# Performance work log

Hardware: AMD Instinct MI355X
Metric: run time of the kernel (lower is better)

## Reference

```python
import jax, jax.numpy as jnp
import numpy as np

N = 20000      # nodes
E = 320000     # edges (before self loops)
HID = 128      # args.hidden
HEADS = 8
C1 = HID // 2  # 64, gat1 out per head -> 512 concat
C2 = HID // 4  # 32, gat2 out per head -> 256 concat
D1 = HEADS * C1  # 512
D2 = HEADS * C2  # 256
JKD = HID + D1 + D2  # 896


def _glorot(key, shape):
    fan_in, fan_out = shape[0], shape[-1]
    s = jnp.sqrt(6.0 / (fan_in + fan_out))
    return jax.random.uniform(key, shape, jnp.float32, -s, s)


def setup_inputs() -> dict:
    key = jax.random.key(0)
    ks = jax.random.split(key, 18)
    x = jax.random.normal(ks[0], (N, HID), jnp.float32)
    edge_index = jax.random.randint(ks[1], (2, E), 0, N, dtype=jnp.int32)
    return {
        "x": x,
        "edge_index": edge_index,
        # GATv2 layer 1
        "Wl1": _glorot(ks[2], (HID, D1)), "bl1": jnp.zeros((D1,), jnp.float32),
        "Wr1": _glorot(ks[3], (HID, D1)), "br1": jnp.zeros((D1,), jnp.float32),
        "att1": _glorot(ks[4], (HEADS, C1)),
        "bias1": jnp.zeros((D1,), jnp.float32),
        # GATv2 layer 2
        "Wl2": _glorot(ks[5], (D1, D2)), "bl2": jnp.zeros((D2,), jnp.float32),
        "Wr2": _glorot(ks[6], (D1, D2)), "br2": jnp.zeros((D2,), jnp.float32),
        "att2": _glorot(ks[7], (HEADS, C2)),
        "bias2": jnp.zeros((D2,), jnp.float32),
        # JK linear
        "Wjk": _glorot(ks[8], (JKD, HID)), "bjk": jnp.zeros((HID,), jnp.float32),
    }


def gatv2_layer(x, src, dst, Wl, bl, Wr, br, att, bias, n):
    """PyG GATv2Conv (concat=True, eval mode: no dropout), neg_slope=0.2."""
    H, C = att.shape
    xl = (x @ Wl + bl).reshape(n, H, C)  # source transform (messages)
    xr = (x @ Wr + br).reshape(n, H, C)  # target transform
    e = jax.nn.leaky_relu(xl[src] + xr[dst], 0.2)        # [E,H,C]
    logits = jnp.einsum('ehc,hc->eh', e, att)            # [E,H]
    # numerically stable segment softmax over incoming edges per dst node
    m = jax.ops.segment_max(logits, dst, num_segments=n) # [N,H]
    a = jnp.exp(logits - m[dst])
    denom = jax.ops.segment_sum(a, dst, num_segments=n)
    alpha = a / denom[dst]                               # [E,H]
    out = jax.ops.segment_sum(alpha[:, :, None] * xl[src], dst, num_segments=n)
    return out.reshape(n, H * C) + bias


def reference(x, edge_index, Wl1, bl1, Wr1, br1, att1, bias1,
              Wl2, bl2, Wr2, br2, att2, bias2, Wjk, bjk):
    n = x.shape[0]
    loop = jnp.arange(n, dtype=edge_index.dtype)
    src = jnp.concatenate([edge_index[0], loop])  # add self loops (PyG default)
    dst = jnp.concatenate([edge_index[1], loop])

    jk0 = x
    h1 = jax.nn.elu(gatv2_layer(x, src, dst, Wl1, bl1, Wr1, br1, att1, bias1, n))
    h2 = jax.nn.elu(gatv2_layer(h1, src, dst, Wl2, bl2, Wr2, br2, att2, bias2, n))
    jk = jnp.concatenate([jk0, h1, h2], axis=-1)  # JumpingKnowledge('cat')
    return jk @ Wjk + bjk
```

## Files before the change

kernel.cpp:

```cpp
#include <hip/hip_runtime.h>

typedef unsigned short u16;
typedef __attribute__((ext_vector_type(8))) short bf16x8;
typedef __attribute__((ext_vector_type(4))) float f32x4;

__device__ __forceinline__ float bf2f(u16 u) { return __uint_as_float(((unsigned)u) << 16); }
__device__ __forceinline__ u16 f2bf(float f) {
  unsigned u = __float_as_uint(f);
  u += 0x7fffu + ((u >> 16) & 1u);
  return (u16)(u >> 16);
}
__device__ __forceinline__ void bf2x2(unsigned w, float& lo, float& hi) {
  lo = __uint_as_float(w << 16);
  hi = __uint_as_float(w & 0xffff0000u);
}

__device__ __forceinline__ float red8(float p) {
  p += __int_as_float(__builtin_amdgcn_ds_swizzle(__float_as_int(p), 0x041F));
  p += __int_as_float(__builtin_amdgcn_ds_swizzle(__float_as_int(p), 0x081F));
  p += __int_as_float(__builtin_amdgcn_ds_swizzle(__float_as_int(p), 0x101F));
  return p;
}

__global__ __launch_bounds__(256) void prep_kernel(
    const float* __restrict__ x,
    const float* __restrict__ bl1, const float* __restrict__ br1,
    const float* __restrict__ bl2, const float* __restrict__ br2,
    u16* __restrict__ XH, float* __restrict__ BC1, float* __restrict__ BC2,
    int* __restrict__ cur,
    int nx, int total)
{
  int i = blockIdx.x * 256 + threadIdx.x;
  if (i >= total) return;
  if (i < nx) { XH[i] = f2bf(x[i]); return; }
  int j = i - nx;
  if (j < 1024) { BC1[j] = (j < 512) ? bl1[j] : br1[j - 512]; return; }
  if (j < 1536) { int t = j - 1024; BC2[t] = (t < 256) ? bl2[t] : br2[t - 256]; return; }
  cur[j - 1536] = 0;
}

__global__ __launch_bounds__(256) void wtrans_kernel(
    const float* __restrict__ Wl1, const float* __restrict__ Wr1,
    const float* __restrict__ Wl2, const float* __restrict__ Wr2,
    const float* __restrict__ Wjk,
    u16* __restrict__ Wp)
{
  __shared__ float T[64][65];
  int t = blockIdx.x;
  const float *Wa, *Wb; int Nhalf, lds, k0, n0, KsT, SUBS; size_t obase; bool split;
  if (t < 32) {
    int kt = t & 1, nt = t >> 1;
    k0 = kt * 64; n0 = nt * 64; obase = 0; KsT = 4; SUBS = 8; split = true;
    Wa = Wl1; Wb = Wr1; Nhalf = 512; lds = 512;
  } else if (t < 96) {
    int tt = t - 32; int kt = tt & 7, nt = tt >> 3;
    k0 = kt * 64; n0 = nt * 64; obase = 262144; KsT = 16; SUBS = 8; split = true;
    Wa = Wl2; Wb = Wr2; Nhalf = 256; lds = 256;
  } else {
    int tt = t - 96; int kt = tt % 14, nt = tt / 14;
    k0 = kt * 64; n0 = nt * 64; obase = 786432; KsT = 28; SUBS = 4; split = false;
    Wa = Wjk; Wb = nullptr; Nhalf = 128; lds = 128;
  }
  const int tid = threadIdx.x;
  const int lane = tid & 63, unit = tid >> 6;
  {
    int n = n0 + lane;
    const float* S = (n < Nhalf) ? Wa : Wb;
    int nn = (n < Nhalf) ? n : n - Nhalf;
#pragma unroll
    for (int r = 0; r < 16; ++r) {
      int kl = unit + 4 * r;
      T[kl][lane] = S[(size_t)(k0 + kl) * lds + nn];
    }
  }
  __syncthreads();
  const int tn = n0 >> 6;
#pragma unroll
  for (int u = 0; u < 2; ++u) {
    int c = unit * 2 + u;
    int ks_l = c >> 2, nc = c & 3;
    int ksg = (k0 >> 5) + ks_l;
    size_t ob = obase + ((size_t)(tn * KsT + ksg) * SUBS + nc) * 512 + lane * 8;
#pragma unroll
    for (int j = 0; j < 8; ++j) {
      float v = T[ks_l * 32 + (lane >> 4) * 8 + j][nc * 16 + (lane & 15)];
      u16 h = f2bf(v);
      Wp[ob + j] = h;
      if (split) Wp[ob + 2048 + j] = f2bf(v - bf2f(h));
    }
  }
}

__global__ __launch_bounds__(256) void hist_kernel(
    const int* __restrict__ ei, int E, int ET, int* __restrict__ cnt)
{
  int e = blockIdx.x * 256 + threadIdx.x;
  if (e >= ET) return;
  int d = (e < E) ? ei[E + e] : (e - E);
  atomicAdd(&cnt[d], 1);
}

__global__ __launch_bounds__(1024) void scan_kernel(
    int* __restrict__ cnt, int* __restrict__ rowptr, int n)
{
  __shared__ int wsum[16];
  __shared__ int carry;
  const int tid = threadIdx.x, lane = tid & 63, wv = tid >> 6;
  if (tid == 0) carry = 0;
  __syncthreads();
  for (int base = 0; base < n; base += 1024) {
    int i = base + tid;
    int v = (i < n) ? cnt[i] : 0;
    if (i < n) cnt[i] = 0;
    int s = v;
#pragma unroll
    for (int ofs = 1; ofs < 64; ofs <<= 1) {
      int t = __shfl_up(s, ofs);
      if (lane >= ofs) s += t;
    }
    if (lane == 63) wsum[wv] = s;
    __syncthreads();
    if (wv == 0 && lane < 16) {
      int t = wsum[lane];
#pragma unroll
      for (int ofs = 1; ofs < 16; ofs <<= 1) {
        int u = __shfl_up(t, ofs);
        if (lane >= ofs) t += u;
      }
      wsum[lane] = t;
    }
    __syncthreads();
    int waveoff = (wv == 0) ? 0 : wsum[wv - 1];
    if (i < n) rowptr[i] = carry + waveoff + s - v;
    int tot = wsum[15];
    __syncthreads();
    if (tid == 0) carry += tot;
    __syncthreads();
  }
  if (threadIdx.x == 0) rowptr[n] = carry;
}

__global__ __launch_bounds__(256) void scatter_kernel(
    const int* __restrict__ ei, int E, int ET,
    const int* __restrict__ rowptr, int* __restrict__ cur, int* __restrict__ srcs)
{
  int e = blockIdx.x * 256 + threadIdx.x;
  if (e >= ET) return;
  int s, d;
  if (e < E) { s = ei[e]; d = ei[E + e]; } else { s = e - E; d = s; }
  int pos = rowptr[d] + atomicAdd(&cur[d], 1);
  srcs[pos] = s;
}

template<int MROWS, int NW, int WPE, bool SPLIT, bool BF16OUT, int LDSU16>
__global__ __launch_bounds__(NW * 64, WPE) void gemmct_kernel(
    const u16* __restrict__ A0, int lda0, int K0,
    const u16* __restrict__ A1, int lda1, int K1,
    const u16* __restrict__ A2, int lda2, int K2,
    const u16* __restrict__ Wp, int KsT,
    int kof0, int kof1, int kof2,
    const float* __restrict__ bias,
    void* __restrict__ Cv, int ldc, int M, int N)
{
  constexpr int SUBS = SPLIT ? 8 : 4;
  __shared__ u16 ldsA[LDSU16];
  const int tid  = threadIdx.x;
  const int lane = tid & 63;
  const int wv   = tid >> 6;
  const int quad = lane >> 4;
  const int r16  = lane & 15;
  const int m0   = blockIdx.x * MROWS;

  const u16* As[3]   = {A0, A1, A2};
  const int  Ks[3]   = {K0, K1, K2};
  const int  ldas[3] = {lda0, lda1, lda2};
  const int  kofs[3] = {kof0, kof1, kof2};

  int soff[3];
  int so = 0;
#pragma unroll
  for (int s = 0; s < 3; ++s) {
    const int K = Ks[s];
    soff[s] = so;
    if (K == 0) continue;
    const int stride = K + 8;
    const int cpr = K >> 3;
    const int sh  = 32 - __clz(cpr - 1);
    const int tot = MROWS << sh;
    for (int c = tid; c < tot; c += NW * 64) {
      int row = c >> sh, kc = c & ((1 << sh) - 1);
      if (kc < cpr) {
        int sr = m0 + row; if (sr >= M) sr = M - 1;
        uint4 v = *reinterpret_cast<const uint4*>(As[s] + (size_t)sr * ldas[s] + kc * 8);
        *reinterpret_cast<uint4*>(&ldsA[so + row * stride + kc * 8]) = v;
      }
    }
    so += MROWS * stride;
  }
  __syncthreads();

  constexpr int MM = MROWS / 16;
  for (int n0w = wv * 64; n0w < N; n0w += NW * 64) {
    const int t = n0w >> 6;
    f32x4 acc[MM][4];
#pragma unroll
    for (int mm = 0; mm < MM; ++mm)
#pragma unroll
      for (int nc = 0; nc < 4; ++nc) acc[mm][nc] = (f32x4){0.f, 0.f, 0.f, 0.f};

#pragma unroll
    for (int s = 0; s < 3; ++s) {
      const int K = Ks[s];
      if (K == 0) continue;
      const int stride = K + 8;
      const int ksb = kofs[s] >> 5;
      const u16* lbase = &ldsA[soff[s] + r16 * stride + quad * 8];

#pragma unroll 2
      for (int k0 = 0; k0 < K; k0 += 32) {
        const int ks = ksb + (k0 >> 5);
        const u16* ch = Wp + (((size_t)(t * KsT + ks) * SUBS) << 9) + lane * 8;
        bf16x8 af[MM];
#pragma unroll
        for (int mm = 0; mm < MM; ++mm)
          af[mm] = *reinterpret_cast<const bf16x8*>(lbase + mm * 16 * stride + k0);
        bf16x8 whf[4], wlf[4];
#pragma unroll
        for (int nc = 0; nc < 4; ++nc) {
          whf[nc] = *reinterpret_cast<const bf16x8*>(ch + (nc << 9));
          if (SPLIT) wlf[nc] = *reinterpret_cast<const bf16x8*>(ch + ((4 + nc) << 9));
        }
#pragma unroll
        for (int mm = 0; mm < MM; ++mm)
#pragma unroll
          for (int nc = 0; nc < 4; ++nc) {
            acc[mm][nc] = __builtin_amdgcn_mfma_f32_16x16x32_bf16(whf[nc], af[mm], acc[mm][nc], 0, 0, 0);
            if (SPLIT)
              acc[mm][nc] = __builtin_amdgcn_mfma_f32_16x16x32_bf16(wlf[nc], af[mm], acc[mm][nc], 0, 0, 0);
          }
      }
    }

#pragma unroll
    for (int mm = 0; mm < MM; ++mm) {
      const int m = m0 + mm * 16 + r16;
      if (m >= M) continue;
#pragma unroll
      for (int nc = 0; nc < 4; ++nc) {
        const int n = n0w + nc * 16 + quad * 4;
        float b0 = 0.f, b1 = 0.f, b2 = 0.f, b3 = 0.f;
        if (bias) {
          float4 bv = *reinterpret_cast<const float4*>(bias + n);
          b0 = bv.x; b1 = bv.y; b2 = bv.z; b3 = bv.w;
        }
        float v0 = acc[mm][nc][0] + b0;
        float v1 = acc[mm][nc][1] + b1;
        float v2 = acc[mm][nc][2] + b2;
        float v3 = acc[mm][nc][3] + b3;
        if (BF16OUT) {
          ushort4 o = { f2bf(v0), f2bf(v1), f2bf(v2), f2bf(v3) };
          *reinterpret_cast<ushort4*>((u16*)Cv + (size_t)m * ldc + n) = o;
        } else {
          float4 o = { v0, v1, v2, v3 };
          *reinterpret_cast<float4*>((float*)Cv + (size_t)m * ldc + n) = o;
        }
      }
    }
  }
}

template<int VPL>
__device__ __forceinline__ void load_row(const u16* p, float* dst) {
  if constexpr (VPL == 8) {
    uint4 t = *reinterpret_cast<const uint4*>(p);
    bf2x2(t.x, dst[0], dst[1]); bf2x2(t.y, dst[2], dst[3]);
    bf2x2(t.z, dst[4], dst[5]); bf2x2(t.w, dst[6], dst[7]);
  } else {
    uint2 t = *reinterpret_cast<const uint2*>(p);
    bf2x2(t.x, dst[0], dst[1]); bf2x2(t.y, dst[2], dst[3]);
  }
}

template<int C>
__global__ __launch_bounds__(256) void gat_node_kernel(
    const u16* __restrict__ XLR,
    const int* __restrict__ rowptr, const int* __restrict__ srcs,
    const float* __restrict__ att, const float* __restrict__ bias,
    u16* __restrict__ Hh, int Nn)
{
  constexpr int D = C * 8;
  constexpr int VPL = D / 64;
  const int lane = threadIdx.x & 63;
  const int wv  = (blockIdx.x * 256 + threadIdx.x) >> 6;
  const int nwv = (gridDim.x * 256) >> 6;

  float c1[VPL], c2[VPL], biasR[VPL];
#pragma unroll
  for (int w = 0; w < VPL; ++w) {
    float a = att[lane * VPL + w];
    c1[w] = 0.6f * a;
    c2[w] = 0.4f * a;
    biasR[w] = bias[lane * VPL + w];
  }

  for (int d = wv; d < Nn; d += nwv) {
    float xr[VPL];
    load_row<VPL>(XLR + (size_t)d * (2 * D) + D + lane * VPL, xr);

    const int jb = rowptr[d], je = rowptr[d + 1];

    float acc[VPL];
    load_row<VPL>(XLR + (size_t)srcs[jb] * (2 * D) + lane * VPL, acc);
    float p0 = 0.f;
#pragma unroll
    for (int w = 0; w < VPL; ++w) {
      float v = acc[w] + xr[w];
      p0 = fmaf(c1[w], v, fmaf(c2[w], fabsf(v), p0));
    }
    p0 = red8(p0);
    float den = 1.f;

    int j = jb + 1;
    for (; j + 5 < je; j += 6) {
      float xs[6][VPL];
      float p[6];
#pragma unroll
      for (int q = 0; q < 6; ++q)
        load_row<VPL>(XLR + (size_t)srcs[j + q] * (2 * D) + lane * VPL, xs[q]);
#pragma unroll
      for (int q = 0; q < 6; ++q) {
        float pp = 0.f;
#pragma unroll
        for (int w = 0; w < VPL; ++w) {
          float v = xs[q][w] + xr[w];
          pp = fmaf(c1[w], v, fmaf(c2[w], fabsf(v), pp));
        }
        p[q] = pp;
      }
#pragma unroll
      for (int q = 0; q < 6; ++q)
        p[q] += __int_as_float(__builtin_amdgcn_ds_swizzle(__float_as_int(p[q]), 0x041F));
#pragma unroll
      for (int q = 0; q < 6; ++q)
        p[q] += __int_as_float(__builtin_amdgcn_ds_swizzle(__float_as_int(p[q]), 0x081F));
#pragma unroll
      for (int q = 0; q < 6; ++q)
        p[q] += __int_as_float(__builtin_amdgcn_ds_swizzle(__float_as_int(p[q]), 0x101F));
      float e[6];
#pragma unroll
      for (int q = 0; q < 6; ++q) e[q] = __expf(p[q] - p0);
      den += ((e[0] + e[1]) + (e[2] + e[3])) + (e[4] + e[5]);
#pragma unroll
      for (int w = 0; w < VPL; ++w) {
        float t0 = fmaf(e[0], xs[0][w], fmaf(e[1], xs[1][w], acc[w]));
        float t1 = fmaf(e[2], xs[2][w], fmaf(e[3], xs[3][w], t0));
        acc[w] = fmaf(e[4], xs[4][w], fmaf(e[5], xs[5][w], t1));
      }
    }
    if (j + 3 < je) {
      float xs[4][VPL];
      float p[4];
#pragma unroll
      for (int q = 0; q < 4; ++q)
        load_row<VPL>(XLR + (size_t)srcs[j + q] * (2 * D) + lane * VPL, xs[q]);
#pragma unroll
      for (int q = 0; q < 4; ++q) {
        float pp = 0.f;
#pragma unroll
        for (int w = 0; w < VPL; ++w) {
          float v = xs[q][w] + xr[w];
          pp = fmaf(c1[w], v, fmaf(c2[w], fabsf(v), pp));
        }
        p[q] = pp;
      }
#pragma unroll
      for (int q = 0; q < 4; ++q)
        p[q] += __int_as_float(__builtin_amdgcn_ds_swizzle(__float_as_int(p[q]), 0x041F));
#pragma unroll
      for (int q = 0; q < 4; ++q)
        p[q] += __int_as_float(__builtin_amdgcn_ds_swizzle(__float_as_int(p[q]), 0x081F));
#pragma unroll
      for (int q = 0; q < 4; ++q)
        p[q] += __int_as_float(__builtin_amdgcn_ds_swizzle(__float_as_int(p[q]), 0x101F));
      float e[4];
#pragma unroll
      for (int q = 0; q < 4; ++q) e[q] = __expf(p[q] - p0);
      den += (e[0] + e[1]) + (e[2] + e[3]);
#pragma unroll
      for (int w = 0; w < VPL; ++w) {
        float t0 = fmaf(e[0], xs[0][w], fmaf(e[1], xs[1][w], acc[w]));
        acc[w] = fmaf(e[2], xs[2][w], fmaf(e[3], xs[3][w], t0));
      }
      j += 4;
    }
    if (j + 1 < je) {
      float xa[VPL], xb[VPL];
      load_row<VPL>(XLR + (size_t)srcs[j]     * (2 * D) + lane * VPL, xa);
      load_row<VPL>(XLR + (size_t)srcs[j + 1] * (2 * D) + lane * VPL, xb);
      float pa = 0.f, pb = 0.f;
#pragma unroll
      for (int w = 0; w < VPL; ++w) {
        float va = xa[w] + xr[w];
        float vb = xb[w] + xr[w];
        pa = fmaf(c1[w], va, fmaf(c2[w], fabsf(va), pa));
        pb = fmaf(c1[w], vb, fmaf(c2[w], fabsf(vb), pb));
      }
      pa = red8(pa); pb = red8(pb);
      const float ea = __expf(pa - p0);
      const float eb = __expf(pb - p0);
      den += ea + eb;
#pragma unroll
      for (int w = 0; w < VPL; ++w)
        acc[w] = fmaf(ea, xa[w], fmaf(eb, xb[w], acc[w]));
      j += 2;
    }
    if (j < je) {
      float xa[VPL];
      load_row<VPL>(XLR + (size_t)srcs[j] * (2 * D) + lane * VPL, xa);
      float pa = 0.f;
#pragma unroll
      for (int w = 0; w < VPL; ++w) {
        float va = xa[w] + xr[w];
        pa = fmaf(c1[w], va, fmaf(c2[w], fabsf(va), pa));
      }
      pa = red8(pa);
      const float ea = __expf(pa - p0);
      den += ea;
#pragma unroll
      for (int w = 0; w < VPL; ++w) acc[w] = fmaf(ea, xa[w], acc[w]);
    }

    const float inv = 1.f / den;
    u16* hh = Hh + (size_t)d * D + lane * VPL;
#pragma unroll
    for (int w = 0; w < VPL; ++w) {
      float v = fmaf(acc[w], inv, biasR[w]);
      v = v > 0.f ? v : (__expf(v) - 1.f);
      hh[w] = f2bf(v);
    }
  }
}


extern "C" void kernel_launch(void* const* d_in, const int* in_sizes, int n_in,
                              void* d_out, int out_size, void* d_ws, size_t ws_size,
                              hipStream_t stream) {
  const float* x     = (const float*)d_in[0];
  const int*   ei    = (const int*)d_in[1];
  const float* Wl1   = (const float*)d_in[2];
  const float* bl1   = (const float*)d_in[3];
  const float* Wr1   = (const float*)d_in[4];
  const float* br1   = (const float*)d_in[5];
  const float* att1  = (const float*)d_in[6];
  const float* bias1 = (const float*)d_in[7];
  const float* Wl2   = (const float*)d_in[8];
  const float* bl2   = (const float*)d_in[9];
  const float* Wr2   = (const float*)d_in[10];
  const float* br2   = (const float*)d_in[11];
  const float* att2  = (const float*)d_in[12];
  const float* bias2 = (const float*)d_in[13];
  const float* Wjk   = (const float*)d_in[14];
  const float* bjk   = (const float*)d_in[15];
  float* out = (float*)d_out;

  const int Nn = in_sizes[0] / 128;
  const int E  = in_sizes[1] / 2;
  const int ET = E + Nn;

  const size_t nx = (size_t)Nn * 128;

  const size_t oW1  = 0;
  const size_t oW2  = 262144;
  const size_t oWjk = 786432;
  const size_t npack = 901120;

  char* ws = (char*)d_ws;
  size_t off = 0;
  u16* XH = (u16*)(ws + off); off += nx * 2;
  u16* Wp = (u16*)(ws + off); off += npack * 2;
  float* BC1 = (float*)(ws + off); off += 1024 * 4;
  float* BC2 = (float*)(ws + off); off += 512 * 4;
  u16* XLR1 = (u16*)(ws + off);
  u16* XLR2 = XLR1;
  off += (size_t)Nn * 1024 * 2;
  u16* H1h = (u16*)(ws + off); off += (size_t)Nn * 512 * 2;
  u16* H2h = (u16*)(ws + off); off += (size_t)Nn * 256 * 2;
  int* rowptr = (int*)(ws + off); off += (size_t)(Nn + 1) * 4;
  int* cur    = (int*)(ws + off); off += (size_t)Nn * 4;
  int* srcs   = (int*)(ws + off); off += (size_t)ET * 4;

  const int nodeblocks = 5000;

  const int nprep = (int)(nx + 1536 + Nn);
  prep_kernel<<<(nprep + 255) / 256, 256, 0, stream>>>(
      x, bl1, br1, bl2, br2, XH, BC1, BC2, cur, (int)nx, nprep);
  wtrans_kernel<<<124, 256, 0, stream>>>(Wl1, Wr1, Wl2, Wr2, Wjk, Wp);
  hist_kernel<<<(ET + 255) / 256, 256, 0, stream>>>(ei, E, ET, cur);
  scan_kernel<<<1, 1024, 0, stream>>>(cur, rowptr, Nn);
  scatter_kernel<<<(ET + 255) / 256, 256, 0, stream>>>(ei, E, ET, rowptr, cur, srcs);

  gemmct_kernel<32, 8, 4, true, true, 32 * 136>
      <<<(Nn + 31) / 32, 512, 0, stream>>>(
      XH, 128, 128, nullptr, 0, 0, nullptr, 0, 0,
      Wp + oW1, 4, 0, 0, 0, BC1,
      XLR1, 1024, Nn, 1024);
  gat_node_kernel<64><<<nodeblocks, 256, 0, stream>>>(
      XLR1, rowptr, srcs, att1, bias1, H1h, Nn);

  gemmct_kernel<48, 8, 4, true, true, 48 * 520>
      <<<(Nn + 47) / 48, 512, 0, stream>>>(
      H1h, 512, 512, nullptr, 0, 0, nullptr, 0, 0,
      Wp + oW2, 16, 0, 0, 0, BC2,
      XLR2, 512, Nn, 512);
  gat_node_kernel<32><<<nodeblocks, 256, 0, stream>>>(
      XLR2, rowptr, srcs, att2, bias2, H2h, Nn);

  gemmct_kernel<16, 2, 1, false, false, 16 * 920>
      <<<(Nn + 15) / 16, 128, 0, stream>>>(
      XH, 128, 128, H1h, 512, 512, H2h, 256, 256,
      Wp + oWjk, 28, 0, 128, 640, bjk,
      out, 128, Nn, 128);
}
```

Before: 312.8 us.

## Split layer-2 GAT wave into two half-waves over edges; vectorize stores; merge prep kernels

The layer-2 GAT node kernel now has each 32-lane half of a wave process alternate incoming edges with 8 bf16 values per lane, using 16-byte loads instead of 8-byte ones. The two halves combine their partial sums with a cross-half shuffle at the end. Both node kernels now write their outputs with packed 16-byte stores. The prep and weight-transpose kernels are merged into a single launch, removing one launch and its serialization.

```diff
diff --git a/kernel.cpp b/kernel.cpp
--- a/kernel.cpp
+++ b/kernel.cpp
@@ -14,6 +14,9 @@
   lo = __uint_as_float(w << 16);
   hi = __uint_as_float(w & 0xffff0000u);
 }
+__device__ __forceinline__ unsigned pk2(float lo, float hi) {
+  return (unsigned)f2bf(lo) | ((unsigned)f2bf(hi) << 16);
+}
 
 __device__ __forceinline__ float red8(float p) {
   p += __int_as_float(__builtin_amdgcn_ds_swizzle(__float_as_int(p), 0x041F));
@@ -21,32 +24,35 @@
   p += __int_as_float(__builtin_amdgcn_ds_swizzle(__float_as_int(p), 0x101F));
   return p;
 }
-
-__global__ __launch_bounds__(256) void prep_kernel(
+__device__ __forceinline__ float red4(float p) {
+  p += __int_as_float(__builtin_amdgcn_ds_swizzle(__float_as_int(p), 0x041F));
+  p += __int_as_float(__builtin_amdgcn_ds_swizzle(__float_as_int(p), 0x081F));
+  return p;
+}
+
+__global__ __launch_bounds__(256) void prepw_kernel(
     const float* __restrict__ x,
     const float* __restrict__ bl1, const float* __restrict__ br1,
     const float* __restrict__ bl2, const float* __restrict__ br2,
-    u16* __restrict__ XH, float* __restrict__ BC1, float* __restrict__ BC2,
-    int* __restrict__ cur,
-    int nx, int total)
-{
-  int i = blockIdx.x * 256 + threadIdx.x;
-  if (i >= total) return;
-  if (i < nx) { XH[i] = f2bf(x[i]); return; }
-  int j = i - nx;
-  if (j < 1024) { BC1[j] = (j < 512) ? bl1[j] : br1[j - 512]; return; }
-  if (j < 1536) { int t = j - 1024; BC2[t] = (t < 256) ? bl2[t] : br2[t - 256]; return; }
-  cur[j - 1536] = 0;
-}
-
-__global__ __launch_bounds__(256) void wtrans_kernel(
     const float* __restrict__ Wl1, const float* __restrict__ Wr1,
     const float* __restrict__ Wl2, const float* __restrict__ Wr2,
     const float* __restrict__ Wjk,
-    u16* __restrict__ Wp)
+    u16* __restrict__ XH, float* __restrict__ BC1, float* __restrict__ BC2,
+    int* __restrict__ cur, u16* __restrict__ Wp,
+    int nx, int total, int prepBlocks)
 {
+  if (blockIdx.x < prepBlocks) {
+    int i = blockIdx.x * 256 + threadIdx.x;
+    if (i >= total) return;
+    if (i < nx) { XH[i] = f2bf(x[i]); return; }
+    int j = i - nx;
+    if (j < 1024) { BC1[j] = (j < 512) ? bl1[j] : br1[j - 512]; return; }
+    if (j < 1536) { int t = j - 1024; BC2[t] = (t < 256) ? bl2[t] : br2[t - 256]; return; }
+    cur[j - 1536] = 0;
+    return;
+  }
   __shared__ float T[64][65];
-  int t = blockIdx.x;
+  int t = blockIdx.x - prepBlocks;
   const float *Wa, *Wb; int Nhalf, lds, k0, n0, KsT, SUBS; size_t obase; bool split;
   if (t < 32) {
     int kt = t & 1, nt = t >> 1;
@@ -281,15 +287,14 @@
   }
 }
 
-template<int C>
-__global__ __launch_bounds__(256) void gat_node_kernel(
+__global__ __launch_bounds__(256) void gat_node1_kernel(
     const u16* __restrict__ XLR,
     const int* __restrict__ rowptr, const int* __restrict__ srcs,
     const float* __restrict__ att, const float* __restrict__ bias,
     u16* __restrict__ Hh, int Nn)
 {
-  constexpr int D = C * 8;
-  constexpr int VPL = D / 64;
+  constexpr int D = 512;
+  constexpr int VPL = 8;
   const int lane = threadIdx.x & 63;
   const int wv  = (blockIdx.x * 256 + threadIdx.x) >> 6;
   const int nwv = (gridDim.x * 256) >> 6;
@@ -431,12 +436,129 @@
     }
 
     const float inv = 1.f / den;
-    u16* hh = Hh + (size_t)d * D + lane * VPL;
+    float o[VPL];
 #pragma unroll
     for (int w = 0; w < VPL; ++w) {
       float v = fmaf(acc[w], inv, biasR[w]);
-      v = v > 0.f ? v : (__expf(v) - 1.f);
-      hh[w] = f2bf(v);
+      o[w] = v > 0.f ? v : (__expf(v) - 1.f);
+    }
+    uint4 ov = { pk2(o[0], o[1]), pk2(o[2], o[3]), pk2(o[4], o[5]), pk2(o[6], o[7]) };
+    *reinterpret_cast<uint4*>(Hh + (size_t)d * D + lane * VPL) = ov;
+  }
+}
+
+__global__ __launch_bounds__(256) void gat_node2_kernel(
+    const u16* __restrict__ XLR,
+    const int* __restrict__ rowptr, const int* __restrict__ srcs,
+    const float* __restrict__ att, const float* __restrict__ bias,
+    u16* __restrict__ Hh, int Nn)
+{
+  constexpr int D = 256;
+  const int lane = threadIdx.x & 63;
+  const int half = lane >> 5;
+  const int l32  = lane & 31;
+  const int wv  = (blockIdx.x * 256 + threadIdx.x) >> 6;
+  const int nwv = (gridDim.x * 256) >> 6;
+
+  float c1[8], c2[8], biasR[8];
+#pragma unroll
+  for (int w = 0; w < 8; ++w) {
+    float a = att[l32 * 8 + w];
+    c1[w] = 0.6f * a;
+    c2[w] = 0.4f * a;
+    biasR[w] = bias[l32 * 8 + w];
+  }
+
+  for (int d = wv; d < Nn; d += nwv) {
+    float xr[8];
+    load_row<8>(XLR + (size_t)d * (2 * D) + D + l32 * 8, xr);
+
+    const int jb = rowptr[d], je = rowptr[d + 1];
+
+    float acc[8];
+    load_row<8>(XLR + (size_t)srcs[jb] * (2 * D) + l32 * 8, acc);
+    float p0 = 0.f;
+#pragma unroll
+    for (int w = 0; w < 8; ++w) {
+      float v = acc[w] + xr[w];
+      p0 = fmaf(c1[w], v, fmaf(c2[w], fabsf(v), p0));
+    }
+    p0 = red4(p0);
+    float den;
+    if (half) {
+      den = 0.f;
+#pragma unroll
+      for (int w = 0; w < 8; ++w) acc[w] = 0.f;
+    } else {
+      den = 1.f;
+    }
+
+    int j = jb + 1;
+    for (; j + 7 < je; j += 8) {
+      float xs[4][8];
+      float p[4];
+#pragma unroll
+      for (int q = 0; q < 4; ++q)
+        load_row<8>(XLR + (size_t)srcs[j + 2 * q + half] * (2 * D) + l32 * 8, xs[q]);
+#pragma unroll
+      for (int q = 0; q < 4; ++q) {
+        float pp = 0.f;
+#pragma unroll
+        for (int w = 0; w < 8; ++w) {
+          float v = xs[q][w] + xr[w];
+          pp = fmaf(c1[w], v, fmaf(c2[w], fabsf(v), pp));
+        }
+        p[q] = pp;
+      }
+#pragma unroll
+      for (int q = 0; q < 4; ++q)
+        p[q] += __int_as_float(__builtin_amdgcn_ds_swizzle(__float_as_int(p[q]), 0x041F));
+#pragma unroll
+      for (int q = 0; q < 4; ++q)
+        p[q] += __int_as_float(__builtin_amdgcn_ds_swizzle(__float_as_int(p[q]), 0x081F));
+      float e[4];
+#pragma unroll
+      for (int q = 0; q < 4; ++q) e[q] = __expf(p[q] - p0);
+      den += (e[0] + e[1]) + (e[2] + e[3]);
+#pragma unroll
+      for (int w = 0; w < 8; ++w) {
+        float t0 = fmaf(e[0], xs[0][w], fmaf(e[1], xs[1][w], acc[w]));
+        acc[w] = fmaf(e[2], xs[2][w], fmaf(e[3], xs[3][w], t0));
+      }
+    }
+    for (; j < je; j += 2) {
+      int jj = j + half;
+      const bool valid = jj < je;
+      if (!valid) jj = je - 1;
+      float xa[8];
+      load_row<8>(XLR + (size_t)srcs[jj] * (2 * D) + l32 * 8, xa);
+      float pa = 0.f;
+#pragma unroll
+      for (int w = 0; w < 8; ++w) {
+        float v = xa[w] + xr[w];
+        pa = fmaf(c1[w], v, fmaf(c2[w], fabsf(v), pa));
+      }
+      pa = red4(pa);
+      const float ea = valid ? __expf(pa - p0) : 0.f;
+      den += ea;
+#pragma unroll
+      for (int w = 0; w < 8; ++w) acc[w] = fmaf(ea, xa[w], acc[w]);
+    }
+
+    den += __shfl_xor(den, 32);
+#pragma unroll
+    for (int w = 0; w < 8; ++w) acc[w] += __shfl_xor(acc[w], 32);
+
+    if (half == 0) {
+      const float inv = 1.f / den;
+      float o[8];
+#pragma unroll
+      for (int w = 0; w < 8; ++w) {
+        float v = fmaf(acc[w], inv, biasR[w]);
+        o[w] = v > 0.f ? v : (__expf(v) - 1.f);
+      }
+      uint4 ov = { pk2(o[0], o[1]), pk2(o[2], o[3]), pk2(o[4], o[5]), pk2(o[6], o[7]) };
+      *reinterpret_cast<uint4*>(Hh + (size_t)d * D + l32 * 8) = ov;
     }
   }
 }
@@ -492,9 +614,10 @@
   const int nodeblocks = 5000;
 
   const int nprep = (int)(nx + 1536 + Nn);
-  prep_kernel<<<(nprep + 255) / 256, 256, 0, stream>>>(
-      x, bl1, br1, bl2, br2, XH, BC1, BC2, cur, (int)nx, nprep);
-  wtrans_kernel<<<124, 256, 0, stream>>>(Wl1, Wr1, Wl2, Wr2, Wjk, Wp);
+  const int prepBlocks = (nprep + 255) / 256;
+  prepw_kernel<<<prepBlocks + 124, 256, 0, stream>>>(
+      x, bl1, br1, bl2, br2, Wl1, Wr1, Wl2, Wr2, Wjk,
+      XH, BC1, BC2, cur, Wp, (int)nx, nprep, prepBlocks);
   hist_kernel<<<(ET + 255) / 256, 256, 0, stream>>>(ei, E, ET, cur);
   scan_kernel<<<1, 1024, 0, stream>>>(cur, rowptr, Nn);
   scatter_kernel<<<(ET + 255) / 256, 256, 0, stream>>>(ei, E, ET, rowptr, cur, srcs);
@@ -504,7 +627,7 @@
       XH, 128, 128, nullptr, 0, 0, nullptr, 0, 0,
       Wp + oW1, 4, 0, 0, 0, BC1,
       XLR1, 1024, Nn, 1024);
-  gat_node_kernel<64><<<nodeblocks, 256, 0, stream>>>(
+  gat_node1_kernel<<<nodeblocks, 256, 0, stream>>>(
       XLR1, rowptr, srcs, att1, bias1, H1h, Nn);
 
   gemmct_kernel<48, 8, 4, true, true, 48 * 520>
@@ -512,7 +635,7 @@
       H1h, 512, 512, nullptr, 0, 0, nullptr, 0, 0,
       Wp + oW2, 16, 0, 0, 0, BC2,
       XLR2, 512, Nn, 512);
-  gat_node_kernel<32><<<nodeblocks, 256, 0, stream>>>(
+  gat_node2_kernel<<<nodeblocks, 256, 0, stream>>>(
       XLR2, rowptr, srcs, att2, bias2, H2h, Nn);
 
   gemmct_kernel<16, 2, 1, false, false, 16 * 920>
```

Result: slower. 320.3 us (+2.4%).
